# Kernel tuning notes

Measured on AMD Instinct MI355X. Metric: run time of the kernel, lower is better.

Reference implementation:

```python
import jax, jax.numpy as jnp
import numpy as np

EPS = 1e-5

def rmsnorm(x, g):
    var = jnp.mean(jnp.square(x), axis=-1, keepdims=True)
    return x * jax.lax.rsqrt(var + EPS) * g

def setup_inputs() -> dict:
    key = jax.random.key(0)
    ks = jax.random.split(key, 8)
    B, S, T, D = 2, 2048, 2048, 1024
    H, HKV, HD = 16, 4, 64
    std = 0.02
    return {
        "x": jax.random.normal(ks[0], (B, S, D), jnp.float32),
        "kv": jax.random.normal(ks[1], (B, T, D), jnp.float32),
        "wq": jax.random.normal(ks[2], (H * HD, D), jnp.float32) * std,
        "wk": jax.random.normal(ks[3], (HKV * HD, D), jnp.float32) * std,
        "wv": jax.random.normal(ks[4], (HKV * HD, D), jnp.float32) * std,
        "wo": jax.random.normal(ks[5], (D, H * HD), jnp.float32) * std,
        "gq": jnp.ones((D,), jnp.float32),
        "gkv": jnp.ones((D,), jnp.float32),
    }

def reference(x, kv, wq, wk, wv, wo, gq, gkv):
    B, S, D = x.shape
    T = kv.shape[1]
    H, HKV, HD = 16, 4, 64
    R = H // HKV  # heads per kv group
    xn = rmsnorm(x, gq)
    kvn = rmsnorm(kv, gkv)
    # projections
    q = (xn @ wq.T).reshape(B, S, HKV, R, HD)   # grouped query heads
    k = (kvn @ wk.T).reshape(B, T, HKV, HD)
    v = (kvn @ wv.T).reshape(B, T, HKV, HD)
    scale = 1.0 / jnp.sqrt(jnp.float32(HD))
    # block-mask is None -> full dense cross attention; GQA via broadcast einsum
    scores = jnp.einsum('bsgrd,btgd->bgrst', q, k) * scale  # [B,HKV,R,S,T]
    probs = jax.nn.softmax(scores, axis=-1)
    out = jnp.einsum('bgrst,btgd->bsgrd', probs, v)  # [B,S,HKV,R,HD]
    out = out.reshape(B, S, H * HD) @ wo.T
    return x + out
```

## Files before the change

kernel.cpp:

```cpp
#include <hip/hip_runtime.h>

#define DEV __device__ __forceinline__

typedef __attribute__((ext_vector_type(8))) _Float16 h8;
typedef __attribute__((ext_vector_type(4))) float f32x4;
typedef __attribute__((ext_vector_type(16))) float f32x16;
typedef __fp16 __attribute__((ext_vector_type(2))) hh2;

DEV unsigned short f2h(float f) {
  union { _Float16 h[2]; unsigned short u[2]; } v;
  v.h[0] = (_Float16)f;
  return v.u[0];
}

DEV float h2f(unsigned short u) {
  union { _Float16 h[2]; unsigned short u[2]; } v;
  v.u[0] = u;
  return (float)v.h[0];
}

DEV void async_load16(const void* g, void* l) {
  __builtin_amdgcn_global_load_lds(
      (const __attribute__((address_space(1))) void*)g,
      (__attribute__((address_space(3))) void*)l,
      16, 0, 0);
}

DEV void pl32swap(unsigned int& a, unsigned int& b) {
  asm("v_permlane32_swap_b32 %0, %1" : "+v"(a), "+v"(b));
}


__global__ __launch_bounds__(256) void prep(const float* __restrict__ x,
                                            const float* __restrict__ kv,
                                            const float* __restrict__ wq,
                                            const float* __restrict__ wk,
                                            const float* __restrict__ wv,
                                            const float* __restrict__ wo,
                                            const float* __restrict__ gq,
                                            const float* __restrict__ gkv,
                                            unsigned short* __restrict__ wqb,
                                            unsigned short* __restrict__ wkvb,
                                            unsigned short* __restrict__ wob,
                                            unsigned short* __restrict__ xn,
                                            unsigned short* __restrict__ kvn,
                                            float qscale) {
  const int b = blockIdx.x, tid = threadIdx.x;
  if (b < 640) {
    const float* src;
    unsigned short* dst;
    float sc = 1.0f;
    int base;
    if (b < 256) { src = wq; dst = wqb; sc = qscale; base = b; }
    else if (b < 320) { src = wk; dst = wkvb; base = b - 256; }
    else if (b < 384) { src = wv; dst = wkvb + 262144; base = b - 320; }
    else { src = wo; dst = wob; base = b - 384; }
#pragma unroll
    for (int j = 0; j < 4; ++j) {
      const int i = base * 4096 + j * 1024 + tid * 4;
      float4 v = *(const float4*)&src[i];
      ushort4 o;
      o.x = f2h(v.x * sc); o.y = f2h(v.y * sc);
      o.z = f2h(v.z * sc); o.w = f2h(v.w * sc);
      *(ushort4*)&dst[i] = o;
    }
    return;
  }
  const int w = tid >> 6, l = tid & 63;
  int row = (b - 640) * 4 + w;
  const float* src;
  const float* g;
  unsigned short* dst;
  if (row < 4096) { src = x; g = gq; dst = xn; }
  else { row -= 4096; src = kv; g = gkv; dst = kvn; }
  const float* xr = src + (size_t)row * 1024;
  float4 v[4];
  float ss = 0.0f;
#pragma unroll
  for (int i = 0; i < 4; ++i) {
    v[i] = *(const float4*)&xr[i * 256 + l * 4];
    ss += v[i].x * v[i].x + v[i].y * v[i].y + v[i].z * v[i].z + v[i].w * v[i].w;
  }
  ss += __shfl_xor(ss, 32); ss += __shfl_xor(ss, 16);
  ss += __shfl_xor(ss, 8);  ss += __shfl_xor(ss, 4);
  ss += __shfl_xor(ss, 2);  ss += __shfl_xor(ss, 1);
  const float inv = rsqrtf(ss * (1.0f / 1024.0f) + 1e-5f);
#pragma unroll
  for (int i = 0; i < 4; ++i) {
    float4 gv = *(const float4*)&g[i * 256 + l * 4];
    ushort4 o;
    o.x = f2h(v[i].x * inv * gv.x); o.y = f2h(v[i].y * inv * gv.y);
    o.z = f2h(v[i].z * inv * gv.z); o.w = f2h(v[i].w * inv * gv.w);
    *(ushort4*)&dst[(size_t)row * 1024 + i * 256 + l * 4] = o;
  }
}

__global__ __launch_bounds__(256, 2) void proj_gemm(const unsigned short* __restrict__ xn,
                                                    const unsigned short* __restrict__ kvn,
                                                    const unsigned short* __restrict__ wqb,
                                                    const unsigned short* __restrict__ wkvb,
                                                    unsigned short* __restrict__ qb,
                                                    unsigned short* __restrict__ kb,
                                                    unsigned short* __restrict__ vTb) {
  __shared__ unsigned short Al[2][2][128 * 32];
  __shared__ unsigned short Bl[2][2][128 * 32];
  const int tid = threadIdx.x;
  const int w = tid >> 6, l = tid & 63;
  const int quad = l >> 4, ln = l & 15;
  const int wm0 = (w >> 1) * 64, wn0 = (w & 1) * 64;
  const int r4 = l >> 2;
  const int c4s = (((l & 3) ^ ((l >> 3) & 3))) * 8;
  const int qs8 = (quad ^ ((l >> 1) & 3)) * 8;

  int z = blockIdx.x;
  const unsigned short *A, *W;
  int m0, n0, isq;
  if (z < 256) {
    A = xn; W = wqb; isq = 1;
    m0 = (((z >> 6) << 3) + (z & 7)) * 128;
    n0 = ((z >> 3) & 7) * 128;
  } else {
    z -= 256; A = kvn; W = wkvb; isq = 0;
    m0 = (((z >> 5) << 3) + (z & 7)) * 128;
    n0 = ((z >> 3) & 3) * 128;
  }

  f32x4 acc[4][4] = {};

  auto stage = [&](int buf, int kk) {
#pragma unroll
    for (int j = 0; j < 8; ++j) {
      const int idx = w * 8 + j;
      if (idx < 16) {
        const int p = idx >> 3, rb = (idx & 7) * 16;
        async_load16(A + (size_t)(m0 + rb + r4) * 1024 + kk + p * 32 + c4s,
                     &Al[buf][p][rb * 32]);
      } else {
        const int ib = idx - 16;
        const int p = ib >> 3, rb = (ib & 7) * 16;
        async_load16(W + (size_t)(n0 + rb + r4) * 1024 + kk + p * 32 + c4s,
                     &Bl[buf][p][rb * 32]);
      }
    }
  };

  stage(0, 0);
  for (int it = 0; it < 16; ++it) {
    const int buf = it & 1;
    __syncthreads();
    if (it < 15) stage(buf ^ 1, (it + 1) * 64);
#pragma unroll
    for (int kc = 0; kc < 2; ++kc) {
      h8 af[4], bf[4];
#pragma unroll
      for (int mi = 0; mi < 4; ++mi)
        af[mi] = *(const h8*)&Al[buf][kc][(wm0 + mi * 16 + ln) * 32 + qs8];
#pragma unroll
      for (int ni = 0; ni < 4; ++ni)
        bf[ni] = *(const h8*)&Bl[buf][kc][(wn0 + ni * 16 + ln) * 32 + qs8];
#pragma unroll
      for (int mi = 0; mi < 4; ++mi)
#pragma unroll
        for (int ni = 0; ni < 4; ++ni)
          acc[mi][ni] = __builtin_amdgcn_mfma_f32_16x16x32_f16(af[mi], bf[ni], acc[mi][ni], 0, 0, 0);
    }
  }

#pragma unroll
  for (int mi = 0; mi < 4; ++mi)
#pragma unroll
    for (int ni = 0; ni < 4; ++ni)
#pragma unroll
      for (int r = 0; r < 4; ++r) {
        const int row = m0 + wm0 + mi * 16 + quad * 4 + r;
        const int col = n0 + wn0 + ni * 16 + ln;
        const unsigned short v = f2h(acc[mi][ni][r]);
        if (isq) {
          qb[((size_t)row << 10) + col] = v;
        } else if (col < 256) {
          kb[(size_t)row * 256 + col] = v;
        } else {
          const int c2 = col - 256, gg = c2 >> 6, dd = c2 & 63;
          const int bb = row >> 11, t = row & 2047;
          vTb[((size_t)((bb * 4 + gg) * 64 + dd) << 11) + t] = v;
        }
      }
}

__global__ __launch_bounds__(256) void o_gemm(const unsigned short* __restrict__ O0,
                                              const unsigned short* __restrict__ O1,
                                              const float* __restrict__ l0p,
                                              const float* __restrict__ l1p,
                                              const unsigned short* __restrict__ wob,
                                              const float* __restrict__ x,
                                              float* __restrict__ out) {
  __shared__ unsigned short Al[2][2][128 * 32];
  __shared__ unsigned short Bl[2][2][128 * 32];
  __shared__ float Linv[16 * 128];
  const int tid = threadIdx.x;
  const int w = tid >> 6, l = tid & 63;
  const int quad = l >> 4, ln = l & 15;
  const int wm0 = (w >> 1) * 64, wn0 = (w & 1) * 64;
  const int r4 = l >> 2;
  const int c4s = (((l & 3) ^ ((l >> 3) & 3))) * 8;
  const int qs8 = (quad ^ ((l >> 1) & 3)) * 8;

  const int z = blockIdx.x;
  const int m0 = (((z >> 6) << 3) + (z & 7)) * 128;
  const int n0 = ((z >> 3) & 7) * 128;

  {
    const int h = tid >> 4, r0 = (tid & 15) * 8;
#pragma unroll
    for (int i = 0; i < 8; ++i) {
      const int r = r0 + i;
      const size_t li = (size_t)(m0 + r) * 16 + h;
      Linv[h * 128 + r] = 1.0f / (l0p[li] + l1p[li]);
    }
  }
  __syncthreads();

  const int srow = tid >> 3;
  const int sp = (tid >> 2) & 1;
  const int ss = tid & 3;

  auto stageA = [&](int buf, int kk) {
    const int h = kk >> 6;
#pragma unroll
    for (int ps = 0; ps < 4; ++ps) {
      const int row = ps * 32 + srow;
      const size_t gidx = (size_t)(m0 + row) * 1024 + kk + sp * 32 + ss * 8;
      h8 a0 = *(const h8*)&O0[gidx];
      h8 a1 = *(const h8*)&O1[gidx];
      const _Float16 lv = (_Float16)Linv[h * 128 + row];
      h8 sum = a0 + a1;
#pragma unroll
      for (int q2 = 0; q2 < 8; ++q2) sum[q2] *= lv;
      const int sl = ss ^ ((row >> 1) & 3);
      *(h8*)&Al[buf][sp][row * 32 + sl * 8] = sum;
    }
  };
  auto stageB = [&](int buf, int kk) {
#pragma unroll
    for (int j = 0; j < 4; ++j) {
      const int ib = w * 4 + j;
      const int p = ib >> 3, rb = (ib & 7) * 16;
      async_load16(wob + (size_t)(n0 + rb + r4) * 1024 + kk + p * 32 + c4s,
                   &Bl[buf][p][rb * 32]);
    }
  };

  f32x4 acc[4][4] = {};
  stageB(0, 0);
  stageA(0, 0);
  for (int it = 0; it < 16; ++it) {
    const int buf = it & 1;
    __syncthreads();
    if (it < 15) { stageB(buf ^ 1, (it + 1) * 64); stageA(buf ^ 1, (it + 1) * 64); }
#pragma unroll
    for (int kc = 0; kc < 2; ++kc) {
      h8 af[4], bf[4];
#pragma unroll
      for (int mi = 0; mi < 4; ++mi)
        af[mi] = *(const h8*)&Al[buf][kc][(wm0 + mi * 16 + ln) * 32 + qs8];
#pragma unroll
      for (int ni = 0; ni < 4; ++ni)
        bf[ni] = *(const h8*)&Bl[buf][kc][(wn0 + ni * 16 + ln) * 32 + qs8];
#pragma unroll
      for (int mi = 0; mi < 4; ++mi)
#pragma unroll
        for (int ni = 0; ni < 4; ++ni)
          acc[mi][ni] = __builtin_amdgcn_mfma_f32_16x16x32_f16(af[mi], bf[ni], acc[mi][ni], 0, 0, 0);
    }
  }

#pragma unroll
  for (int mi = 0; mi < 4; ++mi)
#pragma unroll
    for (int ni = 0; ni < 4; ++ni)
#pragma unroll
      for (int r = 0; r < 4; ++r) {
        const int row = m0 + wm0 + mi * 16 + quad * 4 + r;
        const int col = n0 + wn0 + ni * 16 + ln;
        const size_t idx = ((size_t)row << 10) + col;
        out[idx] = x[idx] + acc[mi][ni][r];
      }
}

__global__ __launch_bounds__(256, 2) void flash_attn(const unsigned short* __restrict__ q,
                                                     const unsigned short* __restrict__ k,
                                                     const unsigned short* __restrict__ vT,
                                                     unsigned short* __restrict__ o0,
                                                     unsigned short* __restrict__ o1,
                                                     float* __restrict__ l0p,
                                                     float* __restrict__ l1p) {
  __shared__ __align__(16) unsigned short Kl[3][64 * 64];
  __shared__ __align__(16) unsigned short Vl[3][64 * 64];

  const int tid = threadIdx.x;
  const int w = tid >> 6, l = tid & 63;
  const int lq = l & 31, hi = l >> 5;
  const int r8 = l >> 3, c8 = l & 7;
  const int csw = (c8 ^ r8) * 8;
  const int rsw = lq & 7;
  const int s0 = blockIdx.x * 256;
  const int h = blockIdx.y, g = h >> 2;
  const int b = blockIdx.z >> 1, ts = blockIdx.z & 1;
  const int tbase = ts << 10;

  unsigned short* Opart = ts ? o1 : o0;
  float* lpart = ts ? l1p : l0p;

  size_t qrow[2];
  qrow[0] = (size_t)(b * 2048 + s0 + w * 64 + lq);
  qrow[1] = qrow[0] + 32;

  h8 qf[2][4];
#pragma unroll
  for (int q2 = 0; q2 < 2; ++q2)
#pragma unroll
    for (int ks = 0; ks < 4; ++ks)
      qf[q2][ks] = *(const h8*)&q[(qrow[q2] << 10) + h * 64 + ks * 16 + hi * 8];
  asm volatile("s_waitcnt vmcnt(0)" ::: "memory");

  int aoff[4];
#pragma unroll
  for (int j = 0; j < 4; ++j)
    aoff[j] = (lq * 64 + (((2 * j + hi) ^ rsw)) * 8) * 2;

  f32x16 oacc[2][2] = {};
  float lsum[2] = {0.0f, 0.0f};

  const unsigned short* kbase = k + ((size_t)(b * 2048)) * 256 + g * 64;
  const unsigned short* vbase = vT + (((size_t)(b * 4 + g) * 64) << 11);

  const hh2 one2 = {(__fp16)1.0f, (__fp16)1.0f};

  auto stage = [&](int sb, int t0) {
#pragma unroll
    for (int j = 0; j < 2; ++j) {
      const int idx = w * 2 + j;
      async_load16(kbase + (size_t)(t0 + idx * 8 + r8) * 256 + csw,
                   &Kl[sb][idx * 512]);
      async_load16(vbase + (((size_t)(idx * 8 + r8)) << 11) + t0 + csw,
                   &Vl[sb][idx * 512]);
    }
  };

#define FA_SYNC(N)                                                   \
  do {                                                               \
    asm volatile("s_waitcnt vmcnt(" #N ")" ::: "memory");            \
    __builtin_amdgcn_s_barrier();                                    \
    __builtin_amdgcn_sched_barrier(0);                               \
  } while (0)

#define FA_HALF(CB, TH)                                                        \
  {                                                                            \
    h8 kf[4];                                                                  \
    _Pragma("unroll")                                                          \
    for (int ks = 0; ks < 4; ++ks)                                             \
      kf[ks] = *(const h8*)((const char*)&Kl[CB][(TH) * 2048] + aoff[ks]);     \
    f32x16 st0 = {}, st1 = {};                                                 \
    __builtin_amdgcn_s_setprio(1);                                             \
    _Pragma("unroll")                                                          \
    for (int ks = 0; ks < 4; ++ks) {                                           \
      st0 = __builtin_amdgcn_mfma_f32_32x32x16_f16(kf[ks], qf[0][ks], st0, 0, 0, 0); \
      st1 = __builtin_amdgcn_mfma_f32_32x32x16_f16(kf[ks], qf[1][ks], st1, 0, 0, 0); \
    }                                                                          \
    __builtin_amdgcn_s_setprio(0);                                             \
    unsigned int w0_[8], w1_[8];                                               \
    _Pragma("unroll")                                                          \
    for (int j = 0; j < 8; ++j) {                                              \
      union { hh2 h2; unsigned int u; } pk0, pk1;                              \
      pk0.h2 = __builtin_amdgcn_cvt_pkrtz(__builtin_amdgcn_exp2f(st0[2 * j]),  \
                                          __builtin_amdgcn_exp2f(st0[2 * j + 1])); \
      pk1.h2 = __builtin_amdgcn_cvt_pkrtz(__builtin_amdgcn_exp2f(st1[2 * j]),  \
                                          __builtin_amdgcn_exp2f(st1[2 * j + 1])); \
      lsum[0] = __builtin_amdgcn_fdot2(pk0.h2, one2, lsum[0], false);          \
      lsum[1] = __builtin_amdgcn_fdot2(pk1.h2, one2, lsum[1], false);          \
      w0_[j] = pk0.u; w1_[j] = pk1.u;                                          \
    }                                                                          \
    h8 pf0[2], pf1[2];                                                         \
    {                                                                          \
      unsigned int a0 = w0_[0], b0 = w0_[2]; pl32swap(a0, b0);                 \
      unsigned int a1 = w0_[1], b1 = w0_[3]; pl32swap(a1, b1);                 \
      unsigned int a4 = w0_[4], b4 = w0_[6]; pl32swap(a4, b4);                 \
      unsigned int a5 = w0_[5], b5 = w0_[7]; pl32swap(a5, b5);                 \
      union { unsigned int u[4]; h8 v; } f0, f1;                               \
      f0.u[0] = a0; f0.u[1] = a1; f0.u[2] = b0; f0.u[3] = b1;                  \
      f1.u[0] = a4; f1.u[1] = a5; f1.u[2] = b4; f1.u[3] = b5;                  \
      pf0[0] = f0.v; pf0[1] = f1.v;                                            \
      unsigned int c0 = w1_[0], d0 = w1_[2]; pl32swap(c0, d0);                 \
      unsigned int c1 = w1_[1], d1 = w1_[3]; pl32swap(c1, d1);                 \
      unsigned int c4 = w1_[4], d4 = w1_[6]; pl32swap(c4, d4);                 \
      unsigned int c5 = w1_[5], d5 = w1_[7]; pl32swap(c5, d5);                 \
      union { unsigned int u[4]; h8 v; } f2, f3;                               \
      f2.u[0] = c0; f2.u[1] = c1; f2.u[2] = d0; f2.u[3] = d1;                  \
      f3.u[0] = c4; f3.u[1] = c5; f3.u[2] = d4; f3.u[3] = d5;                  \
      pf1[0] = f2.v; pf1[1] = f3.v;                                            \
    }                                                                          \
    __builtin_amdgcn_s_setprio(1);                                             \
    _Pragma("unroll")                                                          \
    for (int cc = 0; cc < 2; ++cc) {                                           \
      const int c = (TH) * 2 + cc;                                             \
      h8 v0 = *(const h8*)((const char*)&Vl[CB][0] + aoff[c]);                 \
      h8 v1 = *(const h8*)((const char*)&Vl[CB][2048] + aoff[c]);              \
      oacc[0][0] = __builtin_amdgcn_mfma_f32_32x32x16_f16(v0, pf0[cc], oacc[0][0], 0, 0, 0); \
      oacc[1][0] = __builtin_amdgcn_mfma_f32_32x32x16_f16(v0, pf1[cc], oacc[1][0], 0, 0, 0); \
      oacc[0][1] = __builtin_amdgcn_mfma_f32_32x32x16_f16(v1, pf0[cc], oacc[0][1], 0, 0, 0); \
      oacc[1][1] = __builtin_amdgcn_mfma_f32_32x32x16_f16(v1, pf1[cc], oacc[1][1], 0, 0, 0); \
    }                                                                          \
    __builtin_amdgcn_s_setprio(0);                                             \
  }

#define FA_BODY(CB) { FA_HALF(CB, 0) FA_HALF(CB, 1) }

  stage(0, tbase);
  stage(1, tbase + 64);

  for (int tt = 0; tt < 15; tt += 3) {
    FA_SYNC(4);
    stage(2, tbase + (tt + 2) * 64);
    FA_BODY(0);
    FA_SYNC(4);
    stage(0, tbase + (tt + 3) * 64);
    FA_BODY(1);
    FA_SYNC(4);
    if (tt + 4 < 16) stage(1, tbase + (tt + 4) * 64);
    FA_BODY(2);
  }
  FA_SYNC(0);
  FA_BODY(0);

#undef FA_BODY
#undef FA_HALF
#undef FA_SYNC

#pragma unroll
  for (int q2 = 0; q2 < 2; ++q2) {
    float ls = lsum[q2];
    ls += __shfl_xor(ls, 32);
    if (l < 32) lpart[qrow[q2] * 16 + h] = ls;
#pragma unroll
    for (int dblk = 0; dblk < 2; ++dblk)
#pragma unroll
      for (int qd = 0; qd < 4; ++qd) {
        ushort4 o;
        o.x = f2h(oacc[q2][dblk][qd * 4 + 0]);
        o.y = f2h(oacc[q2][dblk][qd * 4 + 1]);
        o.z = f2h(oacc[q2][dblk][qd * 4 + 2]);
        o.w = f2h(oacc[q2][dblk][qd * 4 + 3]);
        *(ushort4*)&Opart[(qrow[q2] << 10) + h * 64 + dblk * 32 + qd * 8 + hi * 4] = o;
      }
  }
}

extern "C" void kernel_launch(void* const* d_in, const int* in_sizes, int n_in,
                              void* d_out, int out_size, void* d_ws, size_t ws_size,
                              hipStream_t stream) {
  const float* x   = (const float*)d_in[0];
  const float* kv  = (const float*)d_in[1];
  const float* wq  = (const float*)d_in[2];
  const float* wk  = (const float*)d_in[3];
  const float* wv  = (const float*)d_in[4];
  const float* wo  = (const float*)d_in[5];
  const float* gq  = (const float*)d_in[6];
  const float* gkv = (const float*)d_in[7];

  char* ws = (char*)d_ws;
  unsigned short* xn   = (unsigned short*)(ws);
  unsigned short* kvn  = (unsigned short*)(ws + 8388608);
  unsigned short* qb   = (unsigned short*)(ws + 16777216);
  unsigned short* kb   = (unsigned short*)(ws + 25165824);
  unsigned short* vTb  = (unsigned short*)(ws + 27262976);
  unsigned short* wqb  = (unsigned short*)(ws + 37748736);
  unsigned short* wkvb = (unsigned short*)(ws + 39845888);
  unsigned short* wob  = (unsigned short*)(ws + 40894464);
  unsigned short* Opart0 = xn;
  unsigned short* Opart1 = kvn;
  float* l0p = (float*)wqb;
  float* l1p = (float*)(ws + 37748736 + 262144);

  const float qscale = 0.18033688011112042f;

  prep<<<2688, 256, 0, stream>>>(x, kv, wq, wk, wv, wo, gq, gkv,
                                 wqb, wkvb, wob, xn, kvn, qscale);

  proj_gemm<<<384, 256, 0, stream>>>(xn, kvn, wqb, wkvb, qb, kb, vTb);

  flash_attn<<<dim3(8, 16, 4), 256, 0, stream>>>(qb, kb, vTb, Opart0, Opart1, l0p, l1p);

  o_gemm<<<256, 256, 0, stream>>>(Opart0, Opart1, l0p, l1p, wob, x, (float*)d_out);
}
```

Baseline: 190.2 us.

## Triple-buffer proj and output GEMMs with 32-wide K stages and vmcnt barriers

Both projection and output-projection GEMMs move from double-buffered 64-wide K steps to a three-stage ring of 32-wide K slices. Each step waits with a partial vmcnt and a raw s_barrier, so two loads stay in flight behind the MFMA work, and MFMAs run at raised priority. proj_gemm's occupancy hint goes from 2 to 3, and o_gemm now loads the A operand into registers before the MFMAs and writes it to LDS afterward. The aim is to hide global load latency. The cost is more barriers per K, and the hand-written waitcnt logic could race if the counts are wrong.

```diff
diff --git a/kernel.cpp b/kernel.cpp
--- a/kernel.cpp
+++ b/kernel.cpp
@@ -95,15 +95,15 @@
   }
 }
 
-__global__ __launch_bounds__(256, 2) void proj_gemm(const unsigned short* __restrict__ xn,
+__global__ __launch_bounds__(256, 3) void proj_gemm(const unsigned short* __restrict__ xn,
                                                     const unsigned short* __restrict__ kvn,
                                                     const unsigned short* __restrict__ wqb,
                                                     const unsigned short* __restrict__ wkvb,
                                                     unsigned short* __restrict__ qb,
                                                     unsigned short* __restrict__ kb,
                                                     unsigned short* __restrict__ vTb) {
-  __shared__ unsigned short Al[2][2][128 * 32];
-  __shared__ unsigned short Bl[2][2][128 * 32];
+  __shared__ __align__(16) unsigned short Al[3][128 * 32];
+  __shared__ __align__(16) unsigned short Bl[3][128 * 32];
   const int tid = threadIdx.x;
   const int w = tid >> 6, l = tid & 63;
   const int quad = l >> 4, ln = l & 15;
@@ -127,44 +127,66 @@
 
   f32x4 acc[4][4] = {};
 
-  auto stage = [&](int buf, int kk) {
-#pragma unroll
-    for (int j = 0; j < 8; ++j) {
-      const int idx = w * 8 + j;
-      if (idx < 16) {
-        const int p = idx >> 3, rb = (idx & 7) * 16;
-        async_load16(A + (size_t)(m0 + rb + r4) * 1024 + kk + p * 32 + c4s,
-                     &Al[buf][p][rb * 32]);
+  auto stage = [&](int sb, int it) {
+    const int kk = it * 32;
+#pragma unroll
+    for (int j = 0; j < 4; ++j) {
+      const int idx = w * 4 + j;
+      if (idx < 8) {
+        const int rb = idx * 16;
+        async_load16(A + (size_t)(m0 + rb + r4) * 1024 + kk + c4s, &Al[sb][rb * 32]);
       } else {
-        const int ib = idx - 16;
-        const int p = ib >> 3, rb = (ib & 7) * 16;
-        async_load16(W + (size_t)(n0 + rb + r4) * 1024 + kk + p * 32 + c4s,
-                     &Bl[buf][p][rb * 32]);
+        const int rb = (idx - 8) * 16;
+        async_load16(W + (size_t)(n0 + rb + r4) * 1024 + kk + c4s, &Bl[sb][rb * 32]);
       }
     }
   };
 
+#define PJ_SYNC(N)                                                   \
+  do {                                                               \
+    asm volatile("s_waitcnt vmcnt(" #N ")" ::: "memory");            \
+    __builtin_amdgcn_s_barrier();                                    \
+    __builtin_amdgcn_sched_barrier(0);                               \
+  } while (0)
+
+#define PJ_BODY(CB)                                                            \
+  {                                                                            \
+    h8 af[4], bf[4];                                                           \
+    _Pragma("unroll")                                                          \
+    for (int mi = 0; mi < 4; ++mi)                                             \
+      af[mi] = *(const h8*)&Al[CB][(wm0 + mi * 16 + ln) * 32 + qs8];           \
+    _Pragma("unroll")                                                          \
+    for (int ni = 0; ni < 4; ++ni)                                             \
+      bf[ni] = *(const h8*)&Bl[CB][(wn0 + ni * 16 + ln) * 32 + qs8];           \
+    __builtin_amdgcn_s_setprio(1);                                             \
+    _Pragma("unroll")                                                          \
+    for (int mi = 0; mi < 4; ++mi)                                             \
+      _Pragma("unroll")                                                        \
+      for (int ni = 0; ni < 4; ++ni)                                           \
+        acc[mi][ni] = __builtin_amdgcn_mfma_f32_16x16x32_f16(af[mi], bf[ni], acc[mi][ni], 0, 0, 0); \
+    __builtin_amdgcn_s_setprio(0);                                             \
+  }
+
   stage(0, 0);
-  for (int it = 0; it < 16; ++it) {
-    const int buf = it & 1;
-    __syncthreads();
-    if (it < 15) stage(buf ^ 1, (it + 1) * 64);
-#pragma unroll
-    for (int kc = 0; kc < 2; ++kc) {
-      h8 af[4], bf[4];
-#pragma unroll
-      for (int mi = 0; mi < 4; ++mi)
-        af[mi] = *(const h8*)&Al[buf][kc][(wm0 + mi * 16 + ln) * 32 + qs8];
-#pragma unroll
-      for (int ni = 0; ni < 4; ++ni)
-        bf[ni] = *(const h8*)&Bl[buf][kc][(wn0 + ni * 16 + ln) * 32 + qs8];
-#pragma unroll
-      for (int mi = 0; mi < 4; ++mi)
-#pragma unroll
-        for (int ni = 0; ni < 4; ++ni)
-          acc[mi][ni] = __builtin_amdgcn_mfma_f32_16x16x32_f16(af[mi], bf[ni], acc[mi][ni], 0, 0, 0);
-    }
-  }
+  stage(1, 1);
+  for (int tt = 0; tt < 30; tt += 3) {
+    PJ_SYNC(4);
+    stage(2, tt + 2);
+    PJ_BODY(0);
+    PJ_SYNC(4);
+    stage(0, tt + 3);
+    PJ_BODY(1);
+    PJ_SYNC(4);
+    stage(1, tt + 4);
+    PJ_BODY(2);
+  }
+  PJ_SYNC(4);
+  PJ_BODY(0);
+  PJ_SYNC(0);
+  PJ_BODY(1);
+
+#undef PJ_BODY
+#undef PJ_SYNC
 
 #pragma unroll
   for (int mi = 0; mi < 4; ++mi)
@@ -194,8 +216,8 @@
                                               const unsigned short* __restrict__ wob,
                                               const float* __restrict__ x,
                                               float* __restrict__ out) {
-  __shared__ unsigned short Al[2][2][128 * 32];
-  __shared__ unsigned short Bl[2][2][128 * 32];
+  __shared__ __align__(16) unsigned short Al[3][128 * 32];
+  __shared__ __align__(16) unsigned short Bl[3][128 * 32];
   __shared__ float Linv[16 * 128];
   const int tid = threadIdx.x;
   const int w = tid >> 6, l = tid & 63;
@@ -220,59 +242,93 @@
   }
   __syncthreads();
 
-  const int srow = tid >> 3;
-  const int sp = (tid >> 2) & 1;
-  const int ss = tid & 3;
-
-  auto stageA = [&](int buf, int kk) {
-    const int h = kk >> 6;
-#pragma unroll
-    for (int ps = 0; ps < 4; ++ps) {
-      const int row = ps * 32 + srow;
-      const size_t gidx = (size_t)(m0 + row) * 1024 + kk + sp * 32 + ss * 8;
-      h8 a0 = *(const h8*)&O0[gidx];
-      h8 a1 = *(const h8*)&O1[gidx];
-      const _Float16 lv = (_Float16)Linv[h * 128 + row];
-      h8 sum = a0 + a1;
-#pragma unroll
-      for (int q2 = 0; q2 < 8; ++q2) sum[q2] *= lv;
-      const int sl = ss ^ ((row >> 1) & 3);
-      *(h8*)&Al[buf][sp][row * 32 + sl * 8] = sum;
+  const int arow = tid >> 2;
+  const int ac = tid & 3;
+  const int asl = (ac ^ ((arow >> 1) & 3)) * 8;
+
+  auto loadA = [&](int it2, h8* r) {
+    const size_t g0 = (size_t)(m0 + arow) * 1024 + it2 * 32 + ac * 8;
+    const size_t g1 = g0 + (size_t)64 * 1024;
+    r[0] = *(const h8*)&O0[g0];
+    r[1] = *(const h8*)&O1[g0];
+    r[2] = *(const h8*)&O0[g1];
+    r[3] = *(const h8*)&O1[g1];
+  };
+  auto writeA = [&](int sb, int it2, const h8* r) {
+    const int h = it2 >> 1;
+    const _Float16 lv0 = (_Float16)Linv[h * 128 + arow];
+    const _Float16 lv1 = (_Float16)Linv[h * 128 + arow + 64];
+    h8 s0 = r[0] + r[1];
+    h8 s1 = r[2] + r[3];
+#pragma unroll
+    for (int i = 0; i < 8; ++i) { s0[i] *= lv0; s1[i] *= lv1; }
+    *(h8*)&Al[sb][arow * 32 + asl] = s0;
+    *(h8*)&Al[sb][(arow + 64) * 32 + asl] = s1;
+  };
+  auto stageB = [&](int sb, int it2) {
+    const int kk = it2 * 32;
+#pragma unroll
+    for (int j = 0; j < 2; ++j) {
+      const int rb = (w * 2 + j) * 16;
+      async_load16(wob + (size_t)(n0 + rb + r4) * 1024 + kk + c4s, &Bl[sb][rb * 32]);
     }
   };
-  auto stageB = [&](int buf, int kk) {
-#pragma unroll
-    for (int j = 0; j < 4; ++j) {
-      const int ib = w * 4 + j;
-      const int p = ib >> 3, rb = (ib & 7) * 16;
-      async_load16(wob + (size_t)(n0 + rb + r4) * 1024 + kk + p * 32 + c4s,
-                   &Bl[buf][p][rb * 32]);
-    }
-  };
 
   f32x4 acc[4][4] = {};
+
+#define OG_SYNC(N)                                                         \
+  do {                                                                     \
+    asm volatile("s_waitcnt vmcnt(" #N ") lgkmcnt(0)" ::: "memory");       \
+    __builtin_amdgcn_s_barrier();                                          \
+    __builtin_amdgcn_sched_barrier(0);                                     \
+  } while (0)
+
+#define OG_BODY(CB)                                                            \
+  {                                                                            \
+    h8 af[4], bf[4];                                                           \
+    _Pragma("unroll")                                                          \
+    for (int mi = 0; mi < 4; ++mi)                                             \
+      af[mi] = *(const h8*)&Al[CB][(wm0 + mi * 16 + ln) * 32 + qs8];           \
+    _Pragma("unroll")                                                          \
+    for (int ni = 0; ni < 4; ++ni)                                             \
+      bf[ni] = *(const h8*)&Bl[CB][(wn0 + ni * 16 + ln) * 32 + qs8];           \
+    __builtin_amdgcn_s_setprio(1);                                             \
+    _Pragma("unroll")                                                          \
+    for (int mi = 0; mi < 4; ++mi)                                             \
+      _Pragma("unroll")                                                        \
+      for (int ni = 0; ni < 4; ++ni)                                           \
+        acc[mi][ni] = __builtin_amdgcn_mfma_f32_16x16x32_f16(af[mi], bf[ni], acc[mi][ni], 0, 0, 0); \
+    __builtin_amdgcn_s_setprio(0);                                             \
+  }
+
+#define OG_STEP(CUR, NXT, IT2)   \
+  OG_SYNC(2);                    \
+  loadA((IT2), ar);              \
+  stageB(NXT, (IT2));            \
+  OG_BODY(CUR);                  \
+  writeA(NXT, (IT2), ar);
+
+  h8 ar[4], ar2[4];
+  loadA(0, ar);
   stageB(0, 0);
-  stageA(0, 0);
-  for (int it = 0; it < 16; ++it) {
-    const int buf = it & 1;
-    __syncthreads();
-    if (it < 15) { stageB(buf ^ 1, (it + 1) * 64); stageA(buf ^ 1, (it + 1) * 64); }
-#pragma unroll
-    for (int kc = 0; kc < 2; ++kc) {
-      h8 af[4], bf[4];
-#pragma unroll
-      for (int mi = 0; mi < 4; ++mi)
-        af[mi] = *(const h8*)&Al[buf][kc][(wm0 + mi * 16 + ln) * 32 + qs8];
-#pragma unroll
-      for (int ni = 0; ni < 4; ++ni)
-        bf[ni] = *(const h8*)&Bl[buf][kc][(wn0 + ni * 16 + ln) * 32 + qs8];
-#pragma unroll
-      for (int mi = 0; mi < 4; ++mi)
-#pragma unroll
-        for (int ni = 0; ni < 4; ++ni)
-          acc[mi][ni] = __builtin_amdgcn_mfma_f32_16x16x32_f16(af[mi], bf[ni], acc[mi][ni], 0, 0, 0);
-    }
-  }
+  loadA(1, ar2);
+  stageB(1, 1);
+  writeA(0, 0, ar);
+  writeA(1, 1, ar2);
+
+  for (int tt = 0; tt < 30; tt += 3) {
+    OG_STEP(0, 2, tt + 2)
+    OG_STEP(1, 0, tt + 3)
+    OG_STEP(2, 1, tt + 4)
+  }
+  OG_SYNC(2);
+  OG_BODY(0);
+  OG_SYNC(0);
+  OG_BODY(1);
+
+#undef OG_STEP
+#undef OG_BODY
+#undef OG_SYNC
 
 #pragma unroll
   for (int mi = 0; mi < 4; ++mi)
```

New measurement: 196.6 us. 3.4% more time.

## Fuse RMSNorm and fp16 weight conversion into projection and output GEMMs

Applied to the files above, without the earlier changes.

Removes the separate prep kernel. The projection GEMM now loads fp32 activations and weights directly, applies gamma and converts to fp16 in registers before writing LDS, and accumulates the row sum of squares so the RMS scale is applied in the epilogue. The output GEMM likewise converts fp32 wo on the fly, and s_setprio is raised around the MFMA blocks. This saves a launch and the round trips for the fp16 intermediates, but replaces async global-to-LDS loads with synchronous register-staged loads, reads twice as many bytes per tile, and re-converts weights in every block.

```diff
diff --git a/kernel.cpp b/kernel.cpp
--- a/kernel.cpp
+++ b/kernel.cpp
@@ -11,12 +11,6 @@
   union { _Float16 h[2]; unsigned short u[2]; } v;
   v.h[0] = (_Float16)f;
   return v.u[0];
-}
-
-DEV float h2f(unsigned short u) {
-  union { _Float16 h[2]; unsigned short u[2]; } v;
-  v.u[0] = u;
-  return (float)v.h[0];
 }
 
 DEV void async_load16(const void* g, void* l) {
@@ -31,116 +25,81 @@
 }
 
 
-__global__ __launch_bounds__(256) void prep(const float* __restrict__ x,
-                                            const float* __restrict__ kv,
-                                            const float* __restrict__ wq,
-                                            const float* __restrict__ wk,
-                                            const float* __restrict__ wv,
-                                            const float* __restrict__ wo,
-                                            const float* __restrict__ gq,
-                                            const float* __restrict__ gkv,
-                                            unsigned short* __restrict__ wqb,
-                                            unsigned short* __restrict__ wkvb,
-                                            unsigned short* __restrict__ wob,
-                                            unsigned short* __restrict__ xn,
-                                            unsigned short* __restrict__ kvn,
-                                            float qscale) {
-  const int b = blockIdx.x, tid = threadIdx.x;
-  if (b < 640) {
-    const float* src;
-    unsigned short* dst;
-    float sc = 1.0f;
-    int base;
-    if (b < 256) { src = wq; dst = wqb; sc = qscale; base = b; }
-    else if (b < 320) { src = wk; dst = wkvb; base = b - 256; }
-    else if (b < 384) { src = wv; dst = wkvb + 262144; base = b - 320; }
-    else { src = wo; dst = wob; base = b - 384; }
-#pragma unroll
-    for (int j = 0; j < 4; ++j) {
-      const int i = base * 4096 + j * 1024 + tid * 4;
-      float4 v = *(const float4*)&src[i];
-      ushort4 o;
-      o.x = f2h(v.x * sc); o.y = f2h(v.y * sc);
-      o.z = f2h(v.z * sc); o.w = f2h(v.w * sc);
-      *(ushort4*)&dst[i] = o;
-    }
-    return;
-  }
-  const int w = tid >> 6, l = tid & 63;
-  int row = (b - 640) * 4 + w;
-  const float* src;
-  const float* g;
-  unsigned short* dst;
-  if (row < 4096) { src = x; g = gq; dst = xn; }
-  else { row -= 4096; src = kv; g = gkv; dst = kvn; }
-  const float* xr = src + (size_t)row * 1024;
-  float4 v[4];
-  float ss = 0.0f;
-#pragma unroll
-  for (int i = 0; i < 4; ++i) {
-    v[i] = *(const float4*)&xr[i * 256 + l * 4];
-    ss += v[i].x * v[i].x + v[i].y * v[i].y + v[i].z * v[i].z + v[i].w * v[i].w;
-  }
-  ss += __shfl_xor(ss, 32); ss += __shfl_xor(ss, 16);
-  ss += __shfl_xor(ss, 8);  ss += __shfl_xor(ss, 4);
-  ss += __shfl_xor(ss, 2);  ss += __shfl_xor(ss, 1);
-  const float inv = rsqrtf(ss * (1.0f / 1024.0f) + 1e-5f);
-#pragma unroll
-  for (int i = 0; i < 4; ++i) {
-    float4 gv = *(const float4*)&g[i * 256 + l * 4];
-    ushort4 o;
-    o.x = f2h(v[i].x * inv * gv.x); o.y = f2h(v[i].y * inv * gv.y);
-    o.z = f2h(v[i].z * inv * gv.z); o.w = f2h(v[i].w * inv * gv.w);
-    *(ushort4*)&dst[(size_t)row * 1024 + i * 256 + l * 4] = o;
-  }
-}
-
-__global__ __launch_bounds__(256, 2) void proj_gemm(const unsigned short* __restrict__ xn,
-                                                    const unsigned short* __restrict__ kvn,
-                                                    const unsigned short* __restrict__ wqb,
-                                                    const unsigned short* __restrict__ wkvb,
-                                                    unsigned short* __restrict__ qb,
-                                                    unsigned short* __restrict__ kb,
-                                                    unsigned short* __restrict__ vTb) {
-  __shared__ unsigned short Al[2][2][128 * 32];
-  __shared__ unsigned short Bl[2][2][128 * 32];
+__global__ __launch_bounds__(256, 2) void proj_fused(const float* __restrict__ x,
+                                                     const float* __restrict__ kv,
+                                                     const float* __restrict__ wq,
+                                                     const float* __restrict__ wk,
+                                                     const float* __restrict__ wv,
+                                                     const float* __restrict__ gq,
+                                                     const float* __restrict__ gkv,
+                                                     unsigned short* __restrict__ qb,
+                                                     unsigned short* __restrict__ kb,
+                                                     unsigned short* __restrict__ vTb,
+                                                     float qscale) {
+  __shared__ __align__(16) unsigned short Al[2][2][128 * 32];
+  __shared__ __align__(16) unsigned short Bl[2][2][128 * 32];
+  __shared__ float invA[128];
   const int tid = threadIdx.x;
   const int w = tid >> 6, l = tid & 63;
   const int quad = l >> 4, ln = l & 15;
   const int wm0 = (w >> 1) * 64, wn0 = (w & 1) * 64;
-  const int r4 = l >> 2;
-  const int c4s = (((l & 3) ^ ((l >> 3) & 3))) * 8;
   const int qs8 = (quad ^ ((l >> 1) & 3)) * 8;
 
+  const int rA = tid >> 1;
+  const int ch = tid & 1;
+  const int swz = (rA >> 1) & 3;
+
   int z = blockIdx.x;
-  const unsigned short *A, *W;
+  const float *A, *W, *g;
   int m0, n0, isq;
+  float wsc;
   if (z < 256) {
-    A = xn; W = wqb; isq = 1;
+    A = x; g = gq; isq = 1; wsc = qscale;
     m0 = (((z >> 6) << 3) + (z & 7)) * 128;
     n0 = ((z >> 3) & 7) * 128;
+    W = wq + (size_t)n0 * 1024;
   } else {
-    z -= 256; A = kvn; W = wkvb; isq = 0;
+    z -= 256; A = kv; g = gkv; isq = 0; wsc = 1.0f;
     m0 = (((z >> 5) << 3) + (z & 7)) * 128;
     n0 = ((z >> 3) & 3) * 128;
+    W = (n0 < 256) ? (wk + (size_t)n0 * 1024) : (wv + (size_t)(n0 - 256) * 1024);
   }
 
   f32x4 acc[4][4] = {};
-
-  auto stage = [&](int buf, int kk) {
-#pragma unroll
-    for (int j = 0; j < 8; ++j) {
-      const int idx = w * 8 + j;
-      if (idx < 16) {
-        const int p = idx >> 3, rb = (idx & 7) * 16;
-        async_load16(A + (size_t)(m0 + rb + r4) * 1024 + kk + p * 32 + c4s,
-                     &Al[buf][p][rb * 32]);
-      } else {
-        const int ib = idx - 16;
-        const int p = ib >> 3, rb = (ib & 7) * 16;
-        async_load16(W + (size_t)(n0 + rb + r4) * 1024 + kk + p * 32 + c4s,
-                     &Bl[buf][p][rb * 32]);
-      }
+  float ssq = 0.0f;
+
+  auto stage = [&](int sb, int it) {
+    const int kk = it * 64 + ch * 32;
+    const float* ap = A + (size_t)(m0 + rA) * 1024 + kk;
+    const float* bp = W + (size_t)rA * 1024 + kk;
+    const float* gp = g + kk;
+    float4 av[8], bv[8], gv[8];
+#pragma unroll
+    for (int i = 0; i < 8; ++i) av[i] = *(const float4*)(ap + i * 4);
+#pragma unroll
+    for (int i = 0; i < 8; ++i) bv[i] = *(const float4*)(bp + i * 4);
+#pragma unroll
+    for (int i = 0; i < 8; ++i) gv[i] = *(const float4*)(gp + i * 4);
+#pragma unroll
+    for (int i = 0; i < 8; ++i)
+      ssq += av[i].x * av[i].x + av[i].y * av[i].y + av[i].z * av[i].z + av[i].w * av[i].w;
+#pragma unroll
+    for (int cb = 0; cb < 4; ++cb) {
+      float4 a0 = av[2 * cb], a1 = av[2 * cb + 1];
+      float4 g0 = gv[2 * cb], g1 = gv[2 * cb + 1];
+      float4 b0 = bv[2 * cb], b1 = bv[2 * cb + 1];
+      union { hh2 p[4]; h8 v; } ua, ub;
+      ua.p[0] = __builtin_amdgcn_cvt_pkrtz(a0.x * g0.x, a0.y * g0.y);
+      ua.p[1] = __builtin_amdgcn_cvt_pkrtz(a0.z * g0.z, a0.w * g0.w);
+      ua.p[2] = __builtin_amdgcn_cvt_pkrtz(a1.x * g1.x, a1.y * g1.y);
+      ua.p[3] = __builtin_amdgcn_cvt_pkrtz(a1.z * g1.z, a1.w * g1.w);
+      ub.p[0] = __builtin_amdgcn_cvt_pkrtz(b0.x * wsc, b0.y * wsc);
+      ub.p[1] = __builtin_amdgcn_cvt_pkrtz(b0.z * wsc, b0.w * wsc);
+      ub.p[2] = __builtin_amdgcn_cvt_pkrtz(b1.x * wsc, b1.y * wsc);
+      ub.p[3] = __builtin_amdgcn_cvt_pkrtz(b1.z * wsc, b1.w * wsc);
+      const int sl = (cb ^ swz) * 8;
+      *(h8*)&Al[sb][ch][rA * 32 + sl] = ua.v;
+      *(h8*)&Bl[sb][ch][rA * 32 + sl] = ub.v;
     }
   };
 
@@ -148,7 +107,7 @@
   for (int it = 0; it < 16; ++it) {
     const int buf = it & 1;
     __syncthreads();
-    if (it < 15) stage(buf ^ 1, (it + 1) * 64);
+    if (it < 15) stage(buf ^ 1, it + 1);
 #pragma unroll
     for (int kc = 0; kc < 2; ++kc) {
       h8 af[4], bf[4];
@@ -158,13 +117,19 @@
 #pragma unroll
       for (int ni = 0; ni < 4; ++ni)
         bf[ni] = *(const h8*)&Bl[buf][kc][(wn0 + ni * 16 + ln) * 32 + qs8];
+      __builtin_amdgcn_s_setprio(1);
 #pragma unroll
       for (int mi = 0; mi < 4; ++mi)
 #pragma unroll
         for (int ni = 0; ni < 4; ++ni)
           acc[mi][ni] = __builtin_amdgcn_mfma_f32_16x16x32_f16(af[mi], bf[ni], acc[mi][ni], 0, 0, 0);
-    }
-  }
+      __builtin_amdgcn_s_setprio(0);
+    }
+  }
+
+  ssq += __shfl_xor(ssq, 1);
+  if (ch == 0) invA[rA] = rsqrtf(ssq * (1.0f / 1024.0f) + 1e-5f);
+  __syncthreads();
 
 #pragma unroll
   for (int mi = 0; mi < 4; ++mi)
@@ -172,9 +137,10 @@
     for (int ni = 0; ni < 4; ++ni)
 #pragma unroll
       for (int r = 0; r < 4; ++r) {
-        const int row = m0 + wm0 + mi * 16 + quad * 4 + r;
+        const int lr = wm0 + mi * 16 + quad * 4 + r;
+        const int row = m0 + lr;
         const int col = n0 + wn0 + ni * 16 + ln;
-        const unsigned short v = f2h(acc[mi][ni][r]);
+        const unsigned short v = f2h(acc[mi][ni][r] * invA[lr]);
         if (isq) {
           qb[((size_t)row << 10) + col] = v;
         } else if (col < 256) {
@@ -187,22 +153,20 @@
       }
 }
 
-__global__ __launch_bounds__(256) void o_gemm(const unsigned short* __restrict__ O0,
-                                              const unsigned short* __restrict__ O1,
-                                              const float* __restrict__ l0p,
-                                              const float* __restrict__ l1p,
-                                              const unsigned short* __restrict__ wob,
-                                              const float* __restrict__ x,
-                                              float* __restrict__ out) {
-  __shared__ unsigned short Al[2][2][128 * 32];
-  __shared__ unsigned short Bl[2][2][128 * 32];
+__global__ __launch_bounds__(256, 2) void o_fused(const unsigned short* __restrict__ O0,
+                                                  const unsigned short* __restrict__ O1,
+                                                  const float* __restrict__ l0p,
+                                                  const float* __restrict__ l1p,
+                                                  const float* __restrict__ wo,
+                                                  const float* __restrict__ x,
+                                                  float* __restrict__ out) {
+  __shared__ __align__(16) unsigned short Al[2][2][128 * 32];
+  __shared__ __align__(16) unsigned short Bl[2][2][128 * 32];
   __shared__ float Linv[16 * 128];
   const int tid = threadIdx.x;
   const int w = tid >> 6, l = tid & 63;
   const int quad = l >> 4, ln = l & 15;
   const int wm0 = (w >> 1) * 64, wn0 = (w & 1) * 64;
-  const int r4 = l >> 2;
-  const int c4s = (((l & 3) ^ ((l >> 3) & 3))) * 8;
   const int qs8 = (quad ^ ((l >> 1) & 3)) * 8;
 
   const int z = blockIdx.x;
@@ -223,6 +187,9 @@
   const int srow = tid >> 3;
   const int sp = (tid >> 2) & 1;
   const int ss = tid & 3;
+  const int rB = tid >> 1;
+  const int ch = tid & 1;
+  const int swzB = (rB >> 1) & 3;
 
   auto stageA = [&](int buf, int kk) {
     const int h = kk >> 6;
@@ -241,12 +208,19 @@
     }
   };
   auto stageB = [&](int buf, int kk) {
-#pragma unroll
-    for (int j = 0; j < 4; ++j) {
-      const int ib = w * 4 + j;
-      const int p = ib >> 3, rb = (ib & 7) * 16;
-      async_load16(wob + (size_t)(n0 + rb + r4) * 1024 + kk + p * 32 + c4s,
-                   &Bl[buf][p][rb * 32]);
+    const float* bp = wo + (size_t)(n0 + rB) * 1024 + kk + ch * 32;
+    float4 bv[8];
+#pragma unroll
+    for (int i = 0; i < 8; ++i) bv[i] = *(const float4*)(bp + i * 4);
+#pragma unroll
+    for (int cb = 0; cb < 4; ++cb) {
+      float4 b0 = bv[2 * cb], b1 = bv[2 * cb + 1];
+      union { hh2 p[4]; h8 v; } ub;
+      ub.p[0] = __builtin_amdgcn_cvt_pkrtz(b0.x, b0.y);
+      ub.p[1] = __builtin_amdgcn_cvt_pkrtz(b0.z, b0.w);
+      ub.p[2] = __builtin_amdgcn_cvt_pkrtz(b1.x, b1.y);
+      ub.p[3] = __builtin_amdgcn_cvt_pkrtz(b1.z, b1.w);
+      *(h8*)&Bl[buf][ch][rB * 32 + ((cb ^ swzB) * 8)] = ub.v;
     }
   };
 
@@ -266,11 +240,13 @@
 #pragma unroll
       for (int ni = 0; ni < 4; ++ni)
         bf[ni] = *(const h8*)&Bl[buf][kc][(wn0 + ni * 16 + ln) * 32 + qs8];
+      __builtin_amdgcn_s_setprio(1);
 #pragma unroll
       for (int mi = 0; mi < 4; ++mi)
 #pragma unroll
         for (int ni = 0; ni < 4; ++ni)
           acc[mi][ni] = __builtin_amdgcn_mfma_f32_16x16x32_f16(af[mi], bf[ni], acc[mi][ni], 0, 0, 0);
+      __builtin_amdgcn_s_setprio(0);
     }
   }
 
@@ -468,27 +444,19 @@
   const float* gkv = (const float*)d_in[7];
 
   char* ws = (char*)d_ws;
-  unsigned short* xn   = (unsigned short*)(ws);
-  unsigned short* kvn  = (unsigned short*)(ws + 8388608);
-  unsigned short* qb   = (unsigned short*)(ws + 16777216);
-  unsigned short* kb   = (unsigned short*)(ws + 25165824);
-  unsigned short* vTb  = (unsigned short*)(ws + 27262976);
-  unsigned short* wqb  = (unsigned short*)(ws + 37748736);
-  unsigned short* wkvb = (unsigned short*)(ws + 39845888);
-  unsigned short* wob  = (unsigned short*)(ws + 40894464);
-  unsigned short* Opart0 = xn;
-  unsigned short* Opart1 = kvn;
-  float* l0p = (float*)wqb;
-  float* l1p = (float*)(ws + 37748736 + 262144);
+  unsigned short* O0  = (unsigned short*)(ws);
+  unsigned short* O1  = (unsigned short*)(ws + 8388608);
+  unsigned short* qb  = (unsigned short*)(ws + 16777216);
+  unsigned short* kb  = (unsigned short*)(ws + 25165824);
+  unsigned short* vTb = (unsigned short*)(ws + 27262976);
+  float* l0p = (float*)(ws + 37748736);
+  float* l1p = (float*)(ws + 38010880);
 
   const float qscale = 0.18033688011112042f;
 
-  prep<<<2688, 256, 0, stream>>>(x, kv, wq, wk, wv, wo, gq, gkv,
-                                 wqb, wkvb, wob, xn, kvn, qscale);
-
-  proj_gemm<<<384, 256, 0, stream>>>(xn, kvn, wqb, wkvb, qb, kb, vTb);
-
-  flash_attn<<<dim3(8, 16, 4), 256, 0, stream>>>(qb, kb, vTb, Opart0, Opart1, l0p, l1p);
-
-  o_gemm<<<256, 256, 0, stream>>>(Opart0, Opart1, l0p, l1p, wob, x, (float*)d_out);
-}
+  proj_fused<<<384, 256, 0, stream>>>(x, kv, wq, wk, wv, gq, gkv, qb, kb, vTb, qscale);
+
+  flash_attn<<<dim3(8, 16, 4), 256, 0, stream>>>(qb, kb, vTb, O0, O1, l0p, l1p);
+
+  o_fused<<<256, 256, 0, stream>>>(O0, O1, l0p, l1p, wo, x, (float*)d_out);
+}
```

After: 257.1 us. 1.35x slower.

## Split flash attention KV range three ways and raise occupancy hint

Applied to the files above, without the earlier changes.

The attention kernel now splits the 2048-long key/value range into three chunks (11, 11 and 10 tiles of 64) instead of two, giving 768 blocks instead of 512. Launch bounds are raised to 3 blocks per CU so more waves can be resident. The pipelined loop gains guards so it handles the uneven chunk lengths, and the output GEMM now sums three partial O buffers and three partial row sums. The aim is better CU fill and latency hiding, at the cost of extra partial-output traffic and register pressure from the tighter occupancy bound.

```diff
diff --git a/kernel.cpp b/kernel.cpp
--- a/kernel.cpp
+++ b/kernel.cpp
@@ -11,12 +11,6 @@
   union { _Float16 h[2]; unsigned short u[2]; } v;
   v.h[0] = (_Float16)f;
   return v.u[0];
-}
-
-DEV float h2f(unsigned short u) {
-  union { _Float16 h[2]; unsigned short u[2]; } v;
-  v.u[0] = u;
-  return (float)v.h[0];
 }
 
 DEV void async_load16(const void* g, void* l) {
@@ -189,8 +183,10 @@
 
 __global__ __launch_bounds__(256) void o_gemm(const unsigned short* __restrict__ O0,
                                               const unsigned short* __restrict__ O1,
+                                              const unsigned short* __restrict__ O2,
                                               const float* __restrict__ l0p,
                                               const float* __restrict__ l1p,
+                                              const float* __restrict__ l2p,
                                               const unsigned short* __restrict__ wob,
                                               const float* __restrict__ x,
                                               float* __restrict__ out) {
@@ -215,7 +211,7 @@
     for (int i = 0; i < 8; ++i) {
       const int r = r0 + i;
       const size_t li = (size_t)(m0 + r) * 16 + h;
-      Linv[h * 128 + r] = 1.0f / (l0p[li] + l1p[li]);
+      Linv[h * 128 + r] = 1.0f / (l0p[li] + l1p[li] + l2p[li]);
     }
   }
   __syncthreads();
@@ -232,8 +228,9 @@
       const size_t gidx = (size_t)(m0 + row) * 1024 + kk + sp * 32 + ss * 8;
       h8 a0 = *(const h8*)&O0[gidx];
       h8 a1 = *(const h8*)&O1[gidx];
+      h8 a2 = *(const h8*)&O2[gidx];
       const _Float16 lv = (_Float16)Linv[h * 128 + row];
-      h8 sum = a0 + a1;
+      h8 sum = a0 + a1 + a2;
 #pragma unroll
       for (int q2 = 0; q2 < 8; ++q2) sum[q2] *= lv;
       const int sl = ss ^ ((row >> 1) & 3);
@@ -287,13 +284,15 @@
       }
 }
 
-__global__ __launch_bounds__(256, 2) void flash_attn(const unsigned short* __restrict__ q,
+__global__ __launch_bounds__(256, 3) void flash_attn(const unsigned short* __restrict__ q,
                                                      const unsigned short* __restrict__ k,
                                                      const unsigned short* __restrict__ vT,
                                                      unsigned short* __restrict__ o0,
                                                      unsigned short* __restrict__ o1,
+                                                     unsigned short* __restrict__ o2,
                                                      float* __restrict__ l0p,
-                                                     float* __restrict__ l1p) {
+                                                     float* __restrict__ l1p,
+                                                     float* __restrict__ l2p) {
   __shared__ __align__(16) unsigned short Kl[3][64 * 64];
   __shared__ __align__(16) unsigned short Vl[3][64 * 64];
 
@@ -305,11 +304,13 @@
   const int rsw = lq & 7;
   const int s0 = blockIdx.x * 256;
   const int h = blockIdx.y, g = h >> 2;
-  const int b = blockIdx.z >> 1, ts = blockIdx.z & 1;
-  const int tbase = ts << 10;
-
-  unsigned short* Opart = ts ? o1 : o0;
-  float* lpart = ts ? l1p : l0p;
+  const int zz = blockIdx.z;
+  const int b = zz / 3, ts = zz - b * 3;
+  const int nt = (ts == 2) ? 10 : 11;
+  const int tbase = ts * 704;
+
+  unsigned short* Opart = (ts == 0) ? o0 : (ts == 1) ? o1 : o2;
+  float* lpart = (ts == 0) ? l0p : (ts == 1) ? l1p : l2p;
 
   size_t qrow[2];
   qrow[0] = (size_t)(b * 2048 + s0 + w * 64 + lq);
@@ -354,12 +355,12 @@
     __builtin_amdgcn_sched_barrier(0);                               \
   } while (0)
 
-#define FA_HALF(CB, TH)                                                        \
+#define FA_HALF(KB, VB, TH)                                                    \
   {                                                                            \
     h8 kf[4];                                                                  \
     _Pragma("unroll")                                                          \
     for (int ks = 0; ks < 4; ++ks)                                             \
-      kf[ks] = *(const h8*)((const char*)&Kl[CB][(TH) * 2048] + aoff[ks]);     \
+      kf[ks] = *(const h8*)((const char*)(KB) + (TH) * 4096 + aoff[ks]);       \
     f32x16 st0 = {}, st1 = {};                                                 \
     __builtin_amdgcn_s_setprio(1);                                             \
     _Pragma("unroll")                                                          \
@@ -403,8 +404,8 @@
     _Pragma("unroll")                                                          \
     for (int cc = 0; cc < 2; ++cc) {                                           \
       const int c = (TH) * 2 + cc;                                             \
-      h8 v0 = *(const h8*)((const char*)&Vl[CB][0] + aoff[c]);                 \
-      h8 v1 = *(const h8*)((const char*)&Vl[CB][2048] + aoff[c]);              \
+      h8 v0 = *(const h8*)((const char*)(VB) + aoff[c]);                       \
+      h8 v1 = *(const h8*)((const char*)(VB) + 4096 + aoff[c]);                \
       oacc[0][0] = __builtin_amdgcn_mfma_f32_32x32x16_f16(v0, pf0[cc], oacc[0][0], 0, 0, 0); \
       oacc[1][0] = __builtin_amdgcn_mfma_f32_32x32x16_f16(v0, pf1[cc], oacc[1][0], 0, 0, 0); \
       oacc[0][1] = __builtin_amdgcn_mfma_f32_32x32x16_f16(v1, pf0[cc], oacc[0][1], 0, 0, 0); \
@@ -413,24 +414,34 @@
     __builtin_amdgcn_s_setprio(0);                                             \
   }
 
-#define FA_BODY(CB) { FA_HALF(CB, 0) FA_HALF(CB, 1) }
+#define FA_BODY(CB) { FA_HALF(&Kl[CB][0], &Vl[CB][0], 0) FA_HALF(&Kl[CB][0], &Vl[CB][0], 1) }
 
   stage(0, tbase);
   stage(1, tbase + 64);
 
-  for (int tt = 0; tt < 15; tt += 3) {
+  for (int tt = 0; tt + 1 < nt; tt += 3) {
     FA_SYNC(4);
-    stage(2, tbase + (tt + 2) * 64);
+    if (tt + 2 < nt) stage(2, tbase + (tt + 2) * 64);
     FA_BODY(0);
-    FA_SYNC(4);
-    stage(0, tbase + (tt + 3) * 64);
-    FA_BODY(1);
-    FA_SYNC(4);
-    if (tt + 4 < 16) stage(1, tbase + (tt + 4) * 64);
-    FA_BODY(2);
-  }
-  FA_SYNC(0);
-  FA_BODY(0);
+    if (tt + 2 < nt) {
+      FA_SYNC(4);
+      if (tt + 3 < nt) stage(0, tbase + (tt + 3) * 64);
+      FA_BODY(1);
+      if (tt + 3 < nt) {
+        FA_SYNC(4);
+        if (tt + 4 < nt) stage(1, tbase + (tt + 4) * 64);
+        FA_BODY(2);
+      }
+    }
+  }
+  {
+    const int cbt = (ts == 2) ? 0 : 1;
+    const unsigned short* KB = &Kl[cbt][0];
+    const unsigned short* VB = &Vl[cbt][0];
+    FA_SYNC(0);
+    FA_HALF(KB, VB, 0)
+    FA_HALF(KB, VB, 1)
+  }
 
 #undef FA_BODY
 #undef FA_HALF
@@ -473,6 +484,7 @@
   unsigned short* qb   = (unsigned short*)(ws + 16777216);
   unsigned short* kb   = (unsigned short*)(ws + 25165824);
   unsigned short* vTb  = (unsigned short*)(ws + 27262976);
+  unsigned short* O2   = (unsigned short*)(ws + 29360128);
   unsigned short* wqb  = (unsigned short*)(ws + 37748736);
   unsigned short* wkvb = (unsigned short*)(ws + 39845888);
   unsigned short* wob  = (unsigned short*)(ws + 40894464);
@@ -480,6 +492,7 @@
   unsigned short* Opart1 = kvn;
   float* l0p = (float*)wqb;
   float* l1p = (float*)(ws + 37748736 + 262144);
+  float* l2p = (float*)(ws + 37748736 + 524288);
 
   const float qscale = 0.18033688011112042f;
 
@@ -488,7 +501,8 @@
 
   proj_gemm<<<384, 256, 0, stream>>>(xn, kvn, wqb, wkvb, qb, kb, vTb);
 
-  flash_attn<<<dim3(8, 16, 4), 256, 0, stream>>>(qb, kb, vTb, Opart0, Opart1, l0p, l1p);
-
-  o_gemm<<<256, 256, 0, stream>>>(Opart0, Opart1, l0p, l1p, wob, x, (float*)d_out);
-}
+  flash_attn<<<dim3(8, 16, 6), 256, 0, stream>>>(qb, kb, vTb, Opart0, Opart1, O2,
+                                                 l0p, l1p, l2p);
+
+  o_gemm<<<256, 256, 0, stream>>>(Opart0, Opart1, O2, l0p, l1p, l2p, wob, x, (float*)d_out);
+}
```

Result: slower. 225.5 us (+18.6%).
